# Optimization experiments

Hardware: AMD Instinct MI355X
Metric: run time of the kernel (lower is better)

The kernel has to match this reference:

```python
import jax, jax.numpy as jnp
import numpy as np

N = 50000
E = 1600000
IN_C = 165
HID = 256
HEADS = 8
OUT_C = 2
NEG_SLOPE = 0.2


def setup_inputs() -> dict:
    key = jax.random.key(0)
    ks = jax.random.split(key, 10)
    x = jax.random.normal(ks[0], (N, IN_C), dtype=jnp.float32)
    edge_index = jax.random.randint(ks[1], (2, E), 0, N, dtype=jnp.int64)
    c1 = HID // HEADS  # 32 per-head channels in layer 1
    W1 = jax.random.normal(ks[2], (IN_C, HEADS * c1), dtype=jnp.float32) * (1.0 / np.sqrt(IN_C))
    att_src1 = jax.random.normal(ks[3], (HEADS, c1), dtype=jnp.float32) * 0.1
    att_dst1 = jax.random.normal(ks[4], (HEADS, c1), dtype=jnp.float32) * 0.1
    b1 = jnp.zeros((HEADS * c1,), dtype=jnp.float32)
    W2 = jax.random.normal(ks[5], (HID, 1 * OUT_C), dtype=jnp.float32) * (1.0 / np.sqrt(HID))
    att_src2 = jax.random.normal(ks[6], (1, OUT_C), dtype=jnp.float32) * 0.1
    att_dst2 = jax.random.normal(ks[7], (1, OUT_C), dtype=jnp.float32) * 0.1
    b2 = jnp.zeros((OUT_C,), dtype=jnp.float32)
    return {"x": x, "edge_index": edge_index, "W1": W1, "att_src1": att_src1,
            "att_dst1": att_dst1, "b1": b1, "W2": W2, "att_src2": att_src2,
            "att_dst2": att_dst2, "b2": b2}


def _gat_conv(x, src, dst, W, att_src, att_dst, bias, heads, concat):
    """PyG GATConv (eval mode, self-loops already appended to src/dst)."""
    n = x.shape[0]
    c = att_src.shape[1]
    h = (x @ W).reshape(n, heads, c)                      # [N, H, C]
    a_src = jnp.einsum('nhc,hc->nh', h, att_src)          # [N, H]
    a_dst = jnp.einsum('nhc,hc->nh', h, att_dst)
    e = a_src[src] + a_dst[dst]                           # [Et, H]
    e = jax.nn.leaky_relu(e, NEG_SLOPE)
    # segment softmax over incoming edges of each dst node
    e_max = jax.ops.segment_max(e, dst, num_segments=n)   # [N, H]
    e_exp = jnp.exp(e - e_max[dst])
    denom = jax.ops.segment_sum(e_exp, dst, num_segments=n)
    alpha = e_exp / denom[dst]                            # [Et, H]
    msg = alpha[:, :, None] * h[src]                      # [Et, H, C]
    out = jax.ops.segment_sum(msg, dst, num_segments=n)   # [N, H, C]
    if concat:
        out = out.reshape(n, heads * c)
    else:
        out = out.mean(axis=1)
    return out + bias


def reference(x, edge_index, W1, att_src1, att_dst1, b1, W2, att_src2, att_dst2, b2):
    n = x.shape[0]
    loops = jnp.arange(n, dtype=edge_index.dtype)
    src = jnp.concatenate([edge_index[0], loops])  # add_self_loops=True (PyG default)
    dst = jnp.concatenate([edge_index[1], loops])
    h = _gat_conv(x, src, dst, W1, att_src1, att_dst1, b1, HEADS, True)
    h = jax.nn.elu(h)
    out = _gat_conv(h, src, dst, W2, att_src2, att_dst2, b2, 1, False)
    return out
```

## Files before the change

kernel.cpp:

```cpp
#include <hip/hip_runtime.h>
#include <hip/hip_bf16.h>
#include <math.h>

#define N_NODES 50000
#define N_EDGES 1600000
#define ET (N_EDGES + N_NODES)
#define IN_C 165
#define HID 256
#define HEADS 8
#define C1 32
#define OUT_C 2
#define NEG_SLOPE 0.2f
#define TROWS 32
#define XSTR 36
#define GEMM_BLOCKS ((N_NODES + TROWS - 1) / TROWS)
#define NPP ((N_NODES + 7) / 8)
#define CAPL 96
#define GGRP 196
#define SGRP 256
#define TGRP 452
#define NE4 (N_EDGES / 4)

__device__ inline float lrelu(float v) { return v > 0.f ? v : NEG_SLOPE * v; }

__device__ inline unsigned short f32_bf16(float f) {
    unsigned u = __float_as_uint(f);
    return (unsigned short)((u + 0x7FFFu + ((u >> 16) & 1u)) >> 16);
}

__device__ inline float bflo(unsigned u) { return __uint_as_float(u << 16); }
__device__ inline float bfhi(unsigned u) { return __uint_as_float(u & 0xFFFF0000u); }

__device__ __forceinline__ void gemm1_att_block(
        int row0, const float* __restrict__ x, const float* __restrict__ W,
        const float* __restrict__ att_src, const float* __restrict__ att_dst,
        unsigned short* __restrict__ h, float* __restrict__ a_src,
        float* __restrict__ a_dst, float* xs) {
    const int tid = threadIdx.x;
    const int nrow = (N_NODES - row0 < TROWS) ? (N_NODES - row0) : TROWS;
    const int lim = nrow * IN_C;
    for (int idx = tid; idx < TROWS * IN_C; idx += 256) {
        int r = idx / IN_C, k = idx - r * IN_C;
        xs[k * XSTR + r] = (idx < lim) ? x[(size_t)row0 * IN_C + idx] : 0.f;
    }
    __syncthreads();
    const int tr = tid >> 5;
    const int cq = tid & 31;
    const int c0 = cq * 8;
    float acc[4][8];
    #pragma unroll
    for (int j = 0; j < 4; ++j)
        #pragma unroll
        for (int q = 0; q < 8; ++q) acc[j][q] = 0.f;
    float4 xv = *(const float4*)(xs + tr * 4);
    float4 w0 = *(const float4*)(W + c0);
    float4 w1 = *(const float4*)(W + c0 + 4);
    #pragma unroll 3
    for (int k = 0; k < IN_C; ++k) {
        float4 xc = xv, a0 = w0, a1 = w1;
        if (k + 1 < IN_C) {
            xv = *(const float4*)(xs + (k + 1) * XSTR + tr * 4);
            w0 = *(const float4*)(W + (k + 1) * HID + c0);
            w1 = *(const float4*)(W + (k + 1) * HID + c0 + 4);
        }
        #pragma unroll
        for (int j = 0; j < 4; ++j) {
            float xj = (j == 0) ? xc.x : (j == 1) ? xc.y : (j == 2) ? xc.z : xc.w;
            acc[j][0] += xj * a0.x; acc[j][1] += xj * a0.y;
            acc[j][2] += xj * a0.z; acc[j][3] += xj * a0.w;
            acc[j][4] += xj * a1.x; acc[j][5] += xj * a1.y;
            acc[j][6] += xj * a1.z; acc[j][7] += xj * a1.w;
        }
    }
    #pragma unroll
    for (int j = 0; j < 4; ++j) {
        int gr = row0 + tr * 4 + j;
        if (gr < N_NODES) {
            unsigned p[4];
            #pragma unroll
            for (int q = 0; q < 4; ++q)
                p[q] = (unsigned)f32_bf16(acc[j][2*q]) |
                       ((unsigned)f32_bf16(acc[j][2*q+1]) << 16);
            *(uint4*)(h + (size_t)gr * HID + c0) = make_uint4(p[0], p[1], p[2], p[3]);
        }
    }
    {
        const int hd = cq >> 2;
        const float* as = att_src + hd * C1 + (cq & 3) * 8;
        const float* ad = att_dst + hd * C1 + (cq & 3) * 8;
        float av[8], dv[8];
        #pragma unroll
        for (int q = 0; q < 2; ++q) {
            float4 a4 = *(const float4*)(as + q * 4);
            float4 d4 = *(const float4*)(ad + q * 4);
            av[q*4+0]=a4.x; av[q*4+1]=a4.y; av[q*4+2]=a4.z; av[q*4+3]=a4.w;
            dv[q*4+0]=d4.x; dv[q*4+1]=d4.y; dv[q*4+2]=d4.z; dv[q*4+3]=d4.w;
        }
        float ps[4], pd[4];
        #pragma unroll
        for (int j = 0; j < 4; ++j) {
            float s = 0.f, d = 0.f;
            #pragma unroll
            for (int q = 0; q < 8; ++q) {
                s += acc[j][q] * av[q];
                d += acc[j][q] * dv[q];
            }
            ps[j] = s; pd[j] = d;
        }
        #pragma unroll
        for (int off = 1; off <= 2; off <<= 1) {
            #pragma unroll
            for (int j = 0; j < 4; ++j) {
                ps[j] += __shfl_xor(ps[j], off);
                pd[j] += __shfl_xor(pd[j], off);
            }
        }
        if ((cq & 3) == 0) {
            #pragma unroll
            for (int j = 0; j < 4; ++j) {
                int gr = row0 + tr * 4 + j;
                if (gr < N_NODES) {
                    a_src[gr * 8 + hd] = ps[j];
                    a_dst[gr * 8 + hd] = pd[j];
                }
            }
        }
    }
}

__global__ __launch_bounds__(256) void fusedAB_kernel(
        const float* __restrict__ x, const float* __restrict__ W,
        const float* __restrict__ att_src, const float* __restrict__ att_dst,
        unsigned short* __restrict__ h, float* __restrict__ a_src,
        float* __restrict__ a_dst,
        const int* __restrict__ src, const int* __restrict__ dst,
        int* __restrict__ deg, unsigned short* __restrict__ csr) {
    __shared__ float xs[IN_C * XSTR];
    const int g  = blockIdx.x >> 3;
    const int xc = blockIdx.x & 7;
    bool is_gemm;
    int rank;
    if (g < 448) {
        const int hi4 = g >> 4, lo4 = g & 15;
        if (lo4 < 7) { is_gemm = true;  rank = hi4 * 7 + lo4; }
        else         { is_gemm = false; rank = hi4 * 9 + lo4 - 7; }
    } else { is_gemm = false; rank = 252 + (g - 448); }

    if (is_gemm) {
        const int gid = rank * 8 + xc;
        if (gid < GEMM_BLOCKS)
            gemm1_att_block(gid * TROWS, x, W, att_src, att_dst,
                            h, a_src, a_dst, xs);
    } else {
        const int cls = xc;
        const int blk = rank;
        const int lo = cls * NPP;
        const int hi = (lo + NPP < N_NODES) ? lo + NPP : N_NODES;
        const int t = blk * 256 + threadIdx.x;
        if (t < hi - lo) {
            int d = lo + t;
            int slot = atomicAdd(&deg[d], 1);
            csr[(size_t)d * CAPL + slot] = (unsigned short)d;
        }
        const int4* dst4 = (const int4*)dst;
        for (int u = t; u < NE4; u += SGRP * 256) {
            int4 dv = dst4[u];
            #pragma unroll
            for (int j = 0; j < 4; ++j) {
                int d = (j == 0) ? dv.x : (j == 1) ? dv.y : (j == 2) ? dv.z : dv.w;
                if (d >= lo && d < hi) {
                    int slot = atomicAdd(&deg[d], 1);
                    csr[(size_t)d * CAPL + slot] = (unsigned short)src[4 * u + j];
                }
            }
        }
    }
}

__global__ __launch_bounds__(256) void agg1_fused_kernel(
        const int* __restrict__ deg, const unsigned short* __restrict__ csr,
        const float* __restrict__ a_src, const float* __restrict__ a_dst,
        const unsigned short* __restrict__ h1, const float* __restrict__ bias1,
        const float* __restrict__ W2,
        const float* __restrict__ as2, const float* __restrict__ ad2,
        float4* __restrict__ pk, float* __restrict__ a2d) {
    int wid = (blockIdx.x * 256 + threadIdx.x) >> 6;
    int l = threadIdx.x & 63;
    if (wid >= N_NODES) return;
    const int el = l >> 5;
    const int q  = l & 31;
    const int hd = q >> 2;
    const int ch = q * 8;
    const unsigned short* lst = csr + (size_t)wid * CAPL;
    const int n = deg[wid];
    const float ad_p = a_dst[wid * 8 + hd];
    float den = 0.f;
    float acc[8];
    #pragma unroll
    for (int k = 0; k < 8; ++k) acc[k] = 0.f;
    int i = 0;
    for (; i + 16 <= n; i += 16) {
        int s[8];
        #pragma unroll
        for (int j = 0; j < 8; ++j) s[j] = lst[i + 2 * j + el];
        uint4 v[8];
        #pragma unroll
        for (int j = 0; j < 8; ++j)
            v[j] = *(const uint4*)(h1 + (size_t)s[j] * HID + ch);
        float w[8];
        #pragma unroll
        for (int j = 0; j < 8; ++j)
            w[j] = __expf(lrelu(a_src[s[j] * 8 + hd] + ad_p));
        #pragma unroll
        for (int j = 0; j < 8; ++j) {
            den += w[j];
            acc[0] += w[j] * bflo(v[j].x); acc[1] += w[j] * bfhi(v[j].x);
            acc[2] += w[j] * bflo(v[j].y); acc[3] += w[j] * bfhi(v[j].y);
            acc[4] += w[j] * bflo(v[j].z); acc[5] += w[j] * bfhi(v[j].z);
            acc[6] += w[j] * bflo(v[j].w); acc[7] += w[j] * bfhi(v[j].w);
        }
    }
    if (i + 8 <= n) {
        int s[4];
        #pragma unroll
        for (int j = 0; j < 4; ++j) s[j] = lst[i + 2 * j + el];
        uint4 v[4];
        #pragma unroll
        for (int j = 0; j < 4; ++j)
            v[j] = *(const uint4*)(h1 + (size_t)s[j] * HID + ch);
        float w[4];
        #pragma unroll
        for (int j = 0; j < 4; ++j)
            w[j] = __expf(lrelu(a_src[s[j] * 8 + hd] + ad_p));
        #pragma unroll
        for (int j = 0; j < 4; ++j) {
            den += w[j];
            acc[0] += w[j] * bflo(v[j].x); acc[1] += w[j] * bfhi(v[j].x);
            acc[2] += w[j] * bflo(v[j].y); acc[3] += w[j] * bfhi(v[j].y);
            acc[4] += w[j] * bflo(v[j].z); acc[5] += w[j] * bfhi(v[j].z);
            acc[6] += w[j] * bflo(v[j].w); acc[7] += w[j] * bfhi(v[j].w);
        }
        i += 8;
    }
    for (; i < n; i += 2) {
        int e = i + el;
        if (e < n) {
            int s = lst[e];
            uint4 v = *(const uint4*)(h1 + (size_t)s * HID + ch);
            float w = __expf(lrelu(a_src[s * 8 + hd] + ad_p));
            den += w;
            acc[0] += w * bflo(v.x); acc[1] += w * bfhi(v.x);
            acc[2] += w * bflo(v.y); acc[3] += w * bfhi(v.y);
            acc[4] += w * bflo(v.z); acc[5] += w * bfhi(v.z);
            acc[6] += w * bflo(v.w); acc[7] += w * bfhi(v.w);
        }
    }
    den += __shfl_xor(den, 32);
    #pragma unroll
    for (int k = 0; k < 8; ++k) acc[k] += __shfl_xor(acc[k], 32);

    const float inv = 1.f / den;
    float4 bva = *(const float4*)(bias1 + ch);
    float4 bvb = *(const float4*)(bias1 + ch + 4);
    float o[8];
    o[0] = acc[0] * inv + bva.x; o[1] = acc[1] * inv + bva.y;
    o[2] = acc[2] * inv + bva.z; o[3] = acc[3] * inv + bva.w;
    o[4] = acc[4] * inv + bvb.x; o[5] = acc[5] * inv + bvb.y;
    o[6] = acc[6] * inv + bvb.z; o[7] = acc[7] * inv + bvb.w;
    #pragma unroll
    for (int k = 0; k < 8; ++k) o[k] = o[k] > 0.f ? o[k] : expm1f(o[k]);
    const float* wv = W2 + q * 16;
    float4 w0 = *(const float4*)(wv);
    float4 w1 = *(const float4*)(wv + 4);
    float4 w2 = *(const float4*)(wv + 8);
    float4 w3 = *(const float4*)(wv + 12);
    float p0 = o[0]*w0.x + o[1]*w0.z + o[2]*w1.x + o[3]*w1.z
             + o[4]*w2.x + o[5]*w2.z + o[6]*w3.x + o[7]*w3.z;
    float p1 = o[0]*w0.y + o[1]*w0.w + o[2]*w1.y + o[3]*w1.w
             + o[4]*w2.y + o[5]*w2.w + o[6]*w3.y + o[7]*w3.w;
    #pragma unroll
    for (int off = 16; off; off >>= 1) {
        p0 += __shfl_xor(p0, off);
        p1 += __shfl_xor(p1, off);
    }
    if (l == 0) {
        pk[wid] = make_float4(p0, p1, p0 * as2[0] + p1 * as2[1], 0.f);
        a2d[wid] = p0 * ad2[0] + p1 * ad2[1];
    }
}

__global__ __launch_bounds__(256) void agg2_fused_kernel(
        const int* __restrict__ deg, const unsigned short* __restrict__ csr,
        const float4* __restrict__ pk, const float* __restrict__ a2d,
        const float* __restrict__ b2, float* __restrict__ out) {
    int t = blockIdx.x * 256 + threadIdx.x;
    int node = t >> 4;
    int l = t & 15;
    if (node >= N_NODES) return;
    const unsigned short* lst = csr + (size_t)node * CAPL;
    const int n = deg[node];
    const float adv = a2d[node];
    float sm = 0.f, acc0 = 0.f, acc1 = 0.f;
    int i = l;
    for (; i + 16 < n; i += 32) {
        int s0 = lst[i], s1 = lst[i + 16];
        float4 p0 = pk[s0], p1 = pk[s1];
        float w0 = __expf(lrelu(p0.z + adv));
        float w1 = __expf(lrelu(p1.z + adv));
        sm += w0 + w1;
        acc0 += w0 * p0.x + w1 * p1.x;
        acc1 += w0 * p0.y + w1 * p1.y;
    }
    for (; i < n; i += 16) {
        int s = lst[i];
        float4 pv = pk[s];
        float w = __expf(lrelu(pv.z + adv));
        sm += w;
        acc0 += w * pv.x;
        acc1 += w * pv.y;
    }
    #pragma unroll
    for (int off = 8; off; off >>= 1) {
        sm   += __shfl_xor(sm, off);
        acc0 += __shfl_xor(acc0, off);
        acc1 += __shfl_xor(acc1, off);
    }
    if (l == 0) {
        *(float2*)(out + node * 2) =
            make_float2(acc0 / sm + b2[0], acc1 / sm + b2[1]);
    }
}

extern "C" void kernel_launch(void* const* d_in, const int* in_sizes, int n_in,
                              void* d_out, int out_size, void* d_ws, size_t ws_size,
                              hipStream_t stream) {
    (void)in_sizes; (void)n_in; (void)out_size; (void)ws_size;
    const float* x        = (const float*)d_in[0];
    const int*   ei       = (const int*)d_in[1];
    const float* W1       = (const float*)d_in[2];
    const float* att_src1 = (const float*)d_in[3];
    const float* att_dst1 = (const float*)d_in[4];
    const float* b1       = (const float*)d_in[5];
    const float* W2       = (const float*)d_in[6];
    const float* att_src2 = (const float*)d_in[7];
    const float* att_dst2 = (const float*)d_in[8];
    const float* b2       = (const float*)d_in[9];
    float* out = (float*)d_out;

    const int* src = ei;
    const int* dst = ei + N_EDGES;

    char* ws = (char*)d_ws;
    size_t off = 0;
    unsigned short* h1 = (unsigned short*)(ws + off);
    off += (size_t)N_NODES * HID * 2;
    float* a_src1 = (float*)(ws + off); off += (size_t)N_NODES * HEADS * 4;
    float* a_dst1 = (float*)(ws + off); off += (size_t)N_NODES * HEADS * 4;
    float4* pk = (float4*)(ws + off); off += (size_t)N_NODES * 16;
    float* a2d = (float*)(ws + off); off += (size_t)N_NODES * 4;
    int* deg    = (int*)(ws + off); off += (size_t)N_NODES * 4;
    unsigned short* csr = (unsigned short*)(ws + off);
    off += (size_t)N_NODES * CAPL * 2;

    hipMemsetAsync(deg, 0, (size_t)N_NODES * 4, stream);

    const int NW = (N_NODES * 64 + 255) / 256;

    fusedAB_kernel<<<TGRP * 8, 256, 0, stream>>>(
        x, W1, att_src1, att_dst1, h1, a_src1, a_dst1, src, dst, deg, csr);

    agg1_fused_kernel<<<NW, 256, 0, stream>>>(
        deg, csr, a_src1, a_dst1, h1, b1, W2, att_src2, att_dst2, pk, a2d);

    agg2_fused_kernel<<<(N_NODES * 16 + 255) / 256, 256, 0, stream>>>(
        deg, csr, pk, a2d, b2, out);
}
```

Baseline: 345.7 us.

## Stage W1 through double-buffered LDS chunks and simplify block role mapping

The first-layer GEMM now loads W1 in chunks of 8 rows into a double-buffered shared-memory tile, prefetching the next chunk into registers while the current chunk is consumed. This replaces per-thread global W loads on every k. The interleaved GEMM/scatter block assignment is replaced with a simple split: GEMM blocks first, then 2048 CSR-build blocks. The trade is an extra 16KB of LDS per block and a barrier per chunk. The GEMM and scatter work also no longer interleave across the grid.

```diff
diff --git a/kernel.cpp b/kernel.cpp
--- a/kernel.cpp
+++ b/kernel.cpp
@@ -14,12 +14,13 @@
 #define TROWS 32
 #define XSTR 36
 #define GEMM_BLOCKS ((N_NODES + TROWS - 1) / TROWS)
+#define SCB 2048
+#define SGRP 256
 #define NPP ((N_NODES + 7) / 8)
 #define CAPL 96
-#define GGRP 196
-#define SGRP 256
-#define TGRP 452
 #define NE4 (N_EDGES / 4)
+#define CK 8
+#define NCH 21
 
 __device__ inline float lrelu(float v) { return v > 0.f ? v : NEG_SLOPE * v; }
 
@@ -35,7 +36,7 @@
         int row0, const float* __restrict__ x, const float* __restrict__ W,
         const float* __restrict__ att_src, const float* __restrict__ att_dst,
         unsigned short* __restrict__ h, float* __restrict__ a_src,
-        float* __restrict__ a_dst, float* xs) {
+        float* __restrict__ a_dst, float* xs, float* wb) {
     const int tid = threadIdx.x;
     const int nrow = (N_NODES - row0 < TROWS) ? (N_NODES - row0) : TROWS;
     const int lim = nrow * IN_C;
@@ -43,7 +44,17 @@
         int r = idx / IN_C, k = idx - r * IN_C;
         xs[k * XSTR + r] = (idx < lim) ? x[(size_t)row0 * IN_C + idx] : 0.f;
     }
+    const int u  = tid & 31;
+    const int kr = tid >> 5;
+    {
+        const float* ws = W + (size_t)kr * HID + u * 8;
+        float4 pa = *(const float4*)(ws);
+        float4 pb = *(const float4*)(ws + 4);
+        *(float4*)(wb + (kr * 64 + u) * 4)      = pa;
+        *(float4*)(wb + (kr * 64 + u + 32) * 4) = pb;
+    }
     __syncthreads();
+
     const int tr = tid >> 5;
     const int cq = tid & 31;
     const int c0 = cq * 8;
@@ -52,24 +63,51 @@
     for (int j = 0; j < 4; ++j)
         #pragma unroll
         for (int q = 0; q < 8; ++q) acc[j][q] = 0.f;
-    float4 xv = *(const float4*)(xs + tr * 4);
-    float4 w0 = *(const float4*)(W + c0);
-    float4 w1 = *(const float4*)(W + c0 + 4);
-    #pragma unroll 3
-    for (int k = 0; k < IN_C; ++k) {
-        float4 xc = xv, a0 = w0, a1 = w1;
-        if (k + 1 < IN_C) {
-            xv = *(const float4*)(xs + (k + 1) * XSTR + tr * 4);
-            w0 = *(const float4*)(W + (k + 1) * HID + c0);
-            w1 = *(const float4*)(W + (k + 1) * HID + c0 + 4);
-        }
-        #pragma unroll
-        for (int j = 0; j < 4; ++j) {
-            float xj = (j == 0) ? xc.x : (j == 1) ? xc.y : (j == 2) ? xc.z : xc.w;
-            acc[j][0] += xj * a0.x; acc[j][1] += xj * a0.y;
-            acc[j][2] += xj * a0.z; acc[j][3] += xj * a0.w;
-            acc[j][4] += xj * a1.x; acc[j][5] += xj * a1.y;
-            acc[j][6] += xj * a1.z; acc[j][7] += xj * a1.w;
+
+    #pragma unroll 2
+    for (int c = 0; c < NCH - 1; ++c) {
+        int krow = (c + 1) * CK + kr;
+        if (krow > IN_C - 1) krow = IN_C - 1;
+        const float* ws = W + (size_t)krow * HID + u * 8;
+        float4 pa = *(const float4*)(ws);
+        float4 pb = *(const float4*)(ws + 4);
+        const float* wcur = wb + (c & 1) * (CK * 256);
+        const int k0 = c * CK;
+        #pragma unroll
+        for (int kk = 0; kk < CK; ++kk) {
+            float4 xc = *(const float4*)(xs + (k0 + kk) * XSTR + tr * 4);
+            float4 a0 = *(const float4*)(wcur + (kk * 64 + cq) * 4);
+            float4 a1 = *(const float4*)(wcur + (kk * 64 + cq + 32) * 4);
+            #pragma unroll
+            for (int j = 0; j < 4; ++j) {
+                float xj = (j == 0) ? xc.x : (j == 1) ? xc.y : (j == 2) ? xc.z : xc.w;
+                acc[j][0] += xj * a0.x; acc[j][1] += xj * a0.y;
+                acc[j][2] += xj * a0.z; acc[j][3] += xj * a0.w;
+                acc[j][4] += xj * a1.x; acc[j][5] += xj * a1.y;
+                acc[j][6] += xj * a1.z; acc[j][7] += xj * a1.w;
+            }
+        }
+        float* wnxt = wb + ((c + 1) & 1) * (CK * 256);
+        *(float4*)(wnxt + (kr * 64 + u) * 4)      = pa;
+        *(float4*)(wnxt + (kr * 64 + u + 32) * 4) = pb;
+        __syncthreads();
+    }
+    {
+        const float* wcur = wb + ((NCH - 1) & 1) * (CK * 256);
+        const int k0 = (NCH - 1) * CK;
+        #pragma unroll
+        for (int kk = 0; kk < IN_C - (NCH - 1) * CK; ++kk) {
+            float4 xc = *(const float4*)(xs + (k0 + kk) * XSTR + tr * 4);
+            float4 a0 = *(const float4*)(wcur + (kk * 64 + cq) * 4);
+            float4 a1 = *(const float4*)(wcur + (kk * 64 + cq + 32) * 4);
+            #pragma unroll
+            for (int j = 0; j < 4; ++j) {
+                float xj = (j == 0) ? xc.x : (j == 1) ? xc.y : (j == 2) ? xc.z : xc.w;
+                acc[j][0] += xj * a0.x; acc[j][1] += xj * a0.y;
+                acc[j][2] += xj * a0.z; acc[j][3] += xj * a0.w;
+                acc[j][4] += xj * a1.x; acc[j][5] += xj * a1.y;
+                acc[j][6] += xj * a1.z; acc[j][7] += xj * a1.w;
+            }
         }
     }
     #pragma unroll
@@ -136,24 +174,14 @@
         const int* __restrict__ src, const int* __restrict__ dst,
         int* __restrict__ deg, unsigned short* __restrict__ csr) {
     __shared__ float xs[IN_C * XSTR];
-    const int g  = blockIdx.x >> 3;
-    const int xc = blockIdx.x & 7;
-    bool is_gemm;
-    int rank;
-    if (g < 448) {
-        const int hi4 = g >> 4, lo4 = g & 15;
-        if (lo4 < 7) { is_gemm = true;  rank = hi4 * 7 + lo4; }
-        else         { is_gemm = false; rank = hi4 * 9 + lo4 - 7; }
-    } else { is_gemm = false; rank = 252 + (g - 448); }
-
-    if (is_gemm) {
-        const int gid = rank * 8 + xc;
-        if (gid < GEMM_BLOCKS)
-            gemm1_att_block(gid * TROWS, x, W, att_src, att_dst,
-                            h, a_src, a_dst, xs);
+    __shared__ float wlds[2 * CK * 256];
+    if (blockIdx.x < GEMM_BLOCKS) {
+        gemm1_att_block(blockIdx.x * TROWS, x, W, att_src, att_dst,
+                        h, a_src, a_dst, xs, wlds);
     } else {
-        const int cls = xc;
-        const int blk = rank;
+        const int sb  = blockIdx.x - GEMM_BLOCKS;
+        const int cls = sb & 7;
+        const int blk = sb >> 3;
         const int lo = cls * NPP;
         const int hi = (lo + NPP < N_NODES) ? lo + NPP : N_NODES;
         const int t = blk * 256 + threadIdx.x;
@@ -163,14 +191,14 @@
             csr[(size_t)d * CAPL + slot] = (unsigned short)d;
         }
         const int4* dst4 = (const int4*)dst;
-        for (int u = t; u < NE4; u += SGRP * 256) {
-            int4 dv = dst4[u];
+        for (int uu = t; uu < NE4; uu += SGRP * 256) {
+            int4 dv = dst4[uu];
             #pragma unroll
             for (int j = 0; j < 4; ++j) {
                 int d = (j == 0) ? dv.x : (j == 1) ? dv.y : (j == 2) ? dv.z : dv.w;
                 if (d >= lo && d < hi) {
                     int slot = atomicAdd(&deg[d], 1);
-                    csr[(size_t)d * CAPL + slot] = (unsigned short)src[4 * u + j];
+                    csr[(size_t)d * CAPL + slot] = (unsigned short)src[4 * uu + j];
                 }
             }
         }
@@ -366,7 +394,7 @@
 
     const int NW = (N_NODES * 64 + 255) / 256;
 
-    fusedAB_kernel<<<TGRP * 8, 256, 0, stream>>>(
+    fusedAB_kernel<<<GEMM_BLOCKS + SCB, 256, 0, stream>>>(
         x, W1, att_src1, att_dst1, h1, a_src1, a_dst1, src, dst, deg, csr);
 
     agg1_fused_kernel<<<NW, 256, 0, stream>>>(
```

Result: no change. 339.7 us (-1.7%).
